# Kernel optimization log

Hardware: AMD Instinct MI355X
Metric: run time of the kernel (lower is better)

The kernel has to match this reference:

```python
import jax, jax.numpy as jnp
import numpy as np

H = 2048        # hidden_size
NH = 16         # num heads
QLR = 1536      # q_lora_rank
KVLR = 512      # kv_lora_rank
NOPE = 128      # qk_nope_head_dim
ROPE = 64       # qk_rope_head_dim
VH = 128        # v_head_dim
QHD = NOPE + ROPE
EPS = 1e-6
THETA = 10000.0


def rms_norm(x, w):
    x32 = x.astype(jnp.float32)
    inv = jax.lax.rsqrt(jnp.mean(x32 * x32, axis=-1, keepdims=True) + EPS)
    return (x32 * inv * w.astype(jnp.float32)).astype(x.dtype)


def rotate_half(x):
    h = x.shape[-1] // 2
    return jnp.concatenate([-x[..., h:], x[..., :h]], axis=-1)


def setup_inputs() -> dict:
    key = jax.random.key(0)
    ks = jax.random.split(key, 8)
    s = 0.02
    return {
        "hidden_states": jax.random.normal(ks[0], (1, 2048, H), dtype=jnp.float32),
        "q_a_w": jax.random.normal(ks[1], (QLR, H), dtype=jnp.float32) * s,
        "q_a_ln_w": jnp.ones((QLR,), dtype=jnp.float32),
        "q_b_w": jax.random.normal(ks[2], (NH * QHD, QLR), dtype=jnp.float32) * s,
        "kv_a_w": jax.random.normal(ks[3], (KVLR + ROPE, H), dtype=jnp.float32) * s,
        "kv_a_ln_w": jnp.ones((KVLR,), dtype=jnp.float32),
        "kv_b_w": jax.random.normal(ks[4], (NH * (NOPE + VH), KVLR), dtype=jnp.float32) * s,
        "o_w": jax.random.normal(ks[5], (H, NH * VH), dtype=jnp.float32) * s,
    }


def reference(hidden_states, q_a_w, q_a_ln_w, q_b_w, kv_a_w, kv_a_ln_w, kv_b_w, o_w):
    bsz, q_len, _ = hidden_states.shape
    scale = QHD ** -0.5

    # Q path: low-rank down-proj -> RMSNorm -> up-proj
    q_lat = rms_norm(hidden_states @ q_a_w.T, q_a_ln_w)
    q = (q_lat @ q_b_w.T).reshape(bsz, q_len, NH, QHD).transpose(0, 2, 1, 3)  # [B,H,S,QHD]
    q_nope, q_pe = q[..., :NOPE], q[..., NOPE:]

    # KV path: shared latent + decoupled rope key
    kv_lat_pe = hidden_states @ kv_a_w.T
    kv_lat, k_pe = kv_lat_pe[..., :KVLR], kv_lat_pe[..., KVLR:]
    k_pe = k_pe.reshape(bsz, q_len, 1, ROPE).transpose(0, 2, 1, 3)  # [B,1,S,R]
    kv = (rms_norm(kv_lat, kv_a_ln_w) @ kv_b_w.T).reshape(bsz, q_len, NH, NOPE + VH).transpose(0, 2, 1, 3)
    k_nope, v = kv[..., :NOPE], kv[..., NOPE:]

    # RoPE on decoupled sub-dim
    inv_freq = 1.0 / THETA ** (jnp.arange(0, ROPE, 2, dtype=jnp.float32) / ROPE)
    t = jnp.arange(q_len, dtype=jnp.float32)
    freqs = jnp.outer(t, inv_freq)
    emb = jnp.concatenate([freqs, freqs], axis=-1)
    cos = jnp.cos(emb)[None, None]  # [1,1,S,R]
    sin = jnp.sin(emb)[None, None]
    q_pe = q_pe * cos + rotate_half(q_pe) * sin
    k_pe = k_pe * cos + rotate_half(k_pe) * sin

    qs = jnp.concatenate([q_nope, q_pe], axis=-1)                                   # [B,H,S,QHD]
    ks = jnp.concatenate([k_nope, jnp.broadcast_to(k_pe, (bsz, NH, q_len, ROPE))], axis=-1)

    # causal SDPA
    scores = jnp.einsum('bhqd,bhkd->bhqk', qs, ks) * scale
    mask = jnp.tril(jnp.ones((q_len, q_len), dtype=bool))
    scores = jnp.where(mask[None, None], scores, jnp.finfo(scores.dtype).min)
    p = jax.nn.softmax(scores, axis=-1)
    attn = jnp.einsum('bhqk,bhkd->bhqd', p, v)

    attn = attn.transpose(0, 2, 1, 3).reshape(bsz, q_len, NH * VH)
    return attn @ o_w.T
```

## Files before the change

### kernel.cpp

```cpp
#include <hip/hip_runtime.h>
#include <cstdint>

#define H 2048
#define NH 16
#define QLR 1536
#define KVLR 512
#define NOPE 128
#define ROPED 64
#define VH 128
#define QHD 192
#define SEQ 2048
#define NQH (NH*QHD)
#define NKVC (NH*(NOPE+VH))
#define NOV (NH*VH)
#define KVAW_N (KVLR+ROPED)
#define SCALE_L2E 0.10411755f
#define NSEG 4

typedef __attribute__((ext_vector_type(8))) short short8;
typedef __attribute__((ext_vector_type(4))) short short4v;
typedef __attribute__((ext_vector_type(4))) float floatx4;

__device__ __forceinline__ short f2bf(float x) {
  unsigned u = __builtin_bit_cast(unsigned, x);
  unsigned r = (u + 0x7FFFu + ((u >> 16) & 1u)) >> 16;
  return (short)(unsigned short)r;
}
__device__ __forceinline__ float bf2f(short s) {
  unsigned u = ((unsigned)(unsigned short)s) << 16;
  return __builtin_bit_cast(float, u);
}
__device__ __forceinline__ void g2l16(const void* g, void* l) {
  __builtin_amdgcn_global_load_lds(
      (const __attribute__((address_space(1))) void*)(uintptr_t)(g),
      (__attribute__((address_space(3))) void*)(uintptr_t)(l),
      16, 0, 0);
}


struct CvtArgs {
  const float* src[6];
  short* dst[6];
  int cum[7];
};
__global__ __launch_bounds__(256) void k_cvt_all(CvtArgs a, int total4) {
  int stride = gridDim.x * 256;
  for (int i = blockIdx.x * 256 + threadIdx.x; i < total4; i += stride) {
    int j = 0;
#pragma unroll
    for (int t = 1; t < 6; ++t) j += (i >= a.cum[t]);
    int loc = i - a.cum[j];
    float4 v = ((const float4*)a.src[j])[loc];
    short4v o;
    o.x = f2bf(v.x); o.y = f2bf(v.y); o.z = f2bf(v.z); o.w = f2bf(v.w);
    ((short4v*)a.dst[j])[loc] = o;
  }
}

template<int EPI>
__global__ __launch_bounds__(256) void k_gemm128(
    const short* __restrict__ A, const short* __restrict__ B,
    float* __restrict__ C, float* __restrict__ C2, int N, int K)
{
  __shared__ short As[3][4096];
  __shared__ short Bs[3][4096];
  const int tid = threadIdx.x;
  const int lane = tid & 63;
  const int w = tid >> 6;
  const int wm = w & 1, wn = w >> 1;
  const int quad = lane >> 4, l16 = lane & 15;

  const int bid = blockIdx.x;
  const int xcd = bid & 7, j = bid >> 3;
  int mi_, ni_;
  if (EPI == 0) {
    mi_ = (xcd & 3) * 4 + (j & 3);
    ni_ = (xcd >> 2) * 8 + (j >> 2);
  } else {
    mi_ = (xcd & 3) * 4 + (j & 3);
    ni_ = (xcd >> 2) * 9 + (j >> 2);
    if (ni_ >= 17) return;
  }
  const int m0 = mi_ * 128, n0 = ni_ * 128;
  const int T = K >> 5;

  floatx4 acc[4][4] = {};

  auto issue = [&](int t, int buf) {
#pragma unroll
    for (int i = 0; i < 2; ++i) {
      int c = i*256 + tid;
      int row = c & 127, koct = c >> 7;
      g2l16(A + (size_t)(m0 + row)*K + t*32 + koct*8, As[buf] + (koct*128 + row)*8);
      g2l16(B + (size_t)(n0 + row)*K + t*32 + koct*8, Bs[buf] + (koct*128 + row)*8);
    }
  };

  issue(0, 0);
  issue(1, 1);
  int buf = 0;
  for (int t = 0; t < T; ++t) {
    if (t + 2 < T) {
      int nb = buf - 1; if (nb < 0) nb = 2;
      issue(t + 2, nb);
      asm volatile("s_waitcnt vmcnt(8)" ::: "memory");
    } else if (t + 1 < T) {
      asm volatile("s_waitcnt vmcnt(4)" ::: "memory");
    } else {
      asm volatile("s_waitcnt vmcnt(0)" ::: "memory");
    }
    asm volatile("s_barrier" ::: "memory");
    short8 af[4], bfr[4];
#pragma unroll
    for (int mi = 0; mi < 4; ++mi)
      af[mi] = *(const short8*)(As[buf] + (quad*128 + wm*64 + mi*16 + l16)*8);
#pragma unroll
    for (int ni = 0; ni < 4; ++ni)
      bfr[ni] = *(const short8*)(Bs[buf] + (quad*128 + wn*64 + ni*16 + l16)*8);
#pragma unroll
    for (int mi = 0; mi < 4; ++mi)
#pragma unroll
      for (int ni = 0; ni < 4; ++ni)
        acc[mi][ni] = __builtin_amdgcn_mfma_f32_16x16x32_bf16(af[mi], bfr[ni], acc[mi][ni], 0, 0, 0);
    asm volatile("s_barrier" ::: "memory");
    buf = buf + 1; if (buf > 2) buf = 0;
  }

#pragma unroll
  for (int mi = 0; mi < 4; ++mi) {
#pragma unroll
    for (int ni = 0; ni < 4; ++ni) {
      int col = n0 + wn*64 + ni*16 + l16;
#pragma unroll
      for (int r = 0; r < 4; ++r) {
        int row = m0 + wm*64 + mi*16 + quad*4 + r;
        if (EPI == 0) {
          C[(size_t)row*N + col] = acc[mi][ni][r];
        } else {
          if (col < QLR)                C[(size_t)row*QLR + col] = acc[mi][ni][r];
          else if (col < QLR + KVAW_N)  C2[(size_t)row*KVAW_N + (col - QLR)] = acc[mi][ni][r];
        }
      }
    }
  }
}

__global__ __launch_bounds__(256) void k_gemm2(
    const short* __restrict__ qlatn, const short* __restrict__ qbw,
    const short* __restrict__ kvln,  const short* __restrict__ kvbw,
    short* __restrict__ qhm, short* __restrict__ knope, short* __restrict__ vTd)
{
  __shared__ short As[3][4096];
  __shared__ short Bs[3][4096];
  const int tid = threadIdx.x;
  const int lane = tid & 63;
  const int w = tid >> 6;
  const int wm = w & 1, wn = w >> 1;
  const int quad = lane >> 4, l16 = lane & 15;
  int bid = blockIdx.x;
  const short *A, *B; int K, m0, n0; bool isq;
  if (bid < 384) {
    isq = true;  A = qlatn; B = qbw;  K = QLR;
    const int xcd = bid & 7, j = bid >> 3;
    m0 = ((xcd & 3) * 4 + (j & 3)) * 128;
    n0 = ((xcd >> 2) * 12 + (j >> 2)) * 128;
  } else {
    int b2 = bid - 384; isq = false; A = kvln; B = kvbw; K = KVLR;
    const int xcd = b2 & 7, j = b2 >> 3;
    m0 = ((xcd & 3) * 4 + (j & 3)) * 128;
    n0 = ((xcd >> 2) * 16 + (j >> 2)) * 128;
  }
  const int T = K >> 5;

  floatx4 acc[4][4] = {};

  auto issue = [&](int t, int buf) {
#pragma unroll
    for (int i = 0; i < 2; ++i) {
      int c = i*256 + tid;
      int row = c & 127, koct = c >> 7;
      g2l16(A + (size_t)(m0 + row)*K + t*32 + koct*8, As[buf] + (koct*128 + row)*8);
      g2l16(B + (size_t)(n0 + row)*K + t*32 + koct*8, Bs[buf] + (koct*128 + row)*8);
    }
  };

  issue(0, 0);
  issue(1, 1);
  int buf = 0;
  for (int t = 0; t < T; ++t) {
    if (t + 2 < T) {
      int nb = buf - 1; if (nb < 0) nb = 2;
      issue(t + 2, nb);
      asm volatile("s_waitcnt vmcnt(8)" ::: "memory");
    } else if (t + 1 < T) {
      asm volatile("s_waitcnt vmcnt(4)" ::: "memory");
    } else {
      asm volatile("s_waitcnt vmcnt(0)" ::: "memory");
    }
    asm volatile("s_barrier" ::: "memory");
    short8 af[4], bfr[4];
#pragma unroll
    for (int mi = 0; mi < 4; ++mi)
      af[mi] = *(const short8*)(As[buf] + (quad*128 + wm*64 + mi*16 + l16)*8);
#pragma unroll
    for (int ni = 0; ni < 4; ++ni)
      bfr[ni] = *(const short8*)(Bs[buf] + (quad*128 + wn*64 + ni*16 + l16)*8);
#pragma unroll
    for (int mi = 0; mi < 4; ++mi)
#pragma unroll
      for (int ni = 0; ni < 4; ++ni)
        acc[mi][ni] = __builtin_amdgcn_mfma_f32_16x16x32_bf16(af[mi], bfr[ni], acc[mi][ni], 0, 0, 0);
    asm volatile("s_barrier" ::: "memory");
    buf = buf + 1; if (buf > 2) buf = 0;
  }

  const int n064 = n0 + wn * 64;
  if (isq) {
    const int h = n064 / QHD;
    const bool ropew = (n064 % QHD) == 128;
    if (!ropew) {
      const int dbase = n064 - h * QHD;
#pragma unroll
      for (int mi = 0; mi < 4; ++mi) {
        const int qt = (m0 + wm*64 + mi*16) >> 4;
#pragma unroll
        for (int ni = 0; ni < 4; ++ni) {
          int d = dbase + ni*16 + l16;
          size_t tb = ((size_t)(h*128 + qt)*6 + (d>>5))*512
                    + (size_t)(((d>>3)&3)*16)*8 + (d&7);
#pragma unroll
          for (int r = 0; r < 4; ++r)
            qhm[tb + (quad*4 + r)*8] = f2bf(acc[mi][ni][r] * SCALE_L2E);
        }
      }
    } else {
#pragma unroll
      for (int ni = 0; ni < 2; ++ni) {
        int i = ni*16 + l16;
        float fr = powf(10000.0f, -(float)i / 32.0f);
        const int qoff = ((i>>3)*16)*8 + (i&7);
#pragma unroll
        for (int mi = 0; mi < 4; ++mi) {
          const int qt = (m0 + wm*64 + mi*16) >> 4;
          size_t t4 = ((size_t)(h*128 + qt)*6 + 4)*512 + qoff;
#pragma unroll
          for (int r = 0; r < 4; ++r) {
            int row = m0 + wm*64 + mi*16 + quad*4 + r;
            float ang = (float)row * fr;
            float cv, sv; __sincosf(ang, &sv, &cv);
            float x1 = acc[mi][ni][r], x2 = acc[mi][ni+2][r];
            qhm[t4 + (quad*4 + r)*8]       = f2bf((x1*cv - x2*sv) * SCALE_L2E);
            qhm[t4 + 512 + (quad*4 + r)*8] = f2bf((x2*cv + x1*sv) * SCALE_L2E);
          }
        }
      }
    }
  } else {
    const bool isv = (n064 & 128) != 0;
    if (!isv) {
#pragma unroll
      for (int mi = 0; mi < 4; ++mi) {
        const int kt = (m0 + wm*64 + mi*16) >> 4;
#pragma unroll
        for (int ni = 0; ni < 4; ++ni) {
          int col = n064 + ni*16 + l16;
          int hh = col >> 8, d = col & 127;
          size_t tb = ((size_t)(hh*128 + kt)*4 + (d>>5))*512
                    + (size_t)(((d>>3)&3)*16)*8 + (d&7);
#pragma unroll
          for (int r = 0; r < 4; ++r)
            knope[tb + (quad*4 + r)*8] = f2bf(acc[mi][ni][r]);
        }
      }
    } else {
#pragma unroll
      for (int mi = 0; mi < 4; ++mi) {
        const int row0 = m0 + wm*64 + mi*16 + quad*4;
        const int kb = row0 >> 5;
        const int voff = (((row0>>3)&3)*16)*8 + (row0 & 7);
#pragma unroll
        for (int ni = 0; ni < 4; ++ni) {
          int col = n064 + ni*16 + l16;
          int hh = col >> 8, dv = (col & 255) - 128;
          short4v pk;
          pk.x = f2bf(acc[mi][ni][0]); pk.y = f2bf(acc[mi][ni][1]);
          pk.z = f2bf(acc[mi][ni][2]); pk.w = f2bf(acc[mi][ni][3]);
          *(short4v*)(vTd + ((size_t)(hh*8 + (dv>>4))*64 + kb)*512
                          + voff + (dv & 15)*8) = pk;
        }
      }
    }
  }
}

__global__ __launch_bounds__(256) void k_rms2(
    const float* __restrict__ qlat, const float* __restrict__ q_a_ln,
    short* __restrict__ qlatn,
    const float* __restrict__ kvlp, const float* __restrict__ kv_a_ln,
    short* __restrict__ kvln, short* __restrict__ kpe)
{
  int b = blockIdx.x;
  __shared__ float red[4];
  if (b < SEQ) {
    int row = b;
    const float* xr = qlat + (size_t)row * QLR;
    float s = 0.f;
    for (int i = threadIdx.x; i < QLR; i += 256) { float v = xr[i]; s += v*v; }
#pragma unroll
    for (int off = 1; off < 64; off <<= 1) s += __shfl_xor(s, off);
    if ((threadIdx.x & 63) == 0) red[threadIdx.x >> 6] = s;
    __syncthreads();
    float inv = rsqrtf((red[0]+red[1]+red[2]+red[3]) / (float)QLR + 1e-6f);
    for (int i = threadIdx.x; i < QLR; i += 256)
      qlatn[(size_t)row * QLR + i] = f2bf(xr[i] * inv * q_a_ln[i]);
  } else {
    int row = b - SEQ;
    const float* xr = kvlp + (size_t)row * KVAW_N;
    float s = 0.f;
    for (int i = threadIdx.x; i < KVLR; i += 256) { float v = xr[i]; s += v*v; }
#pragma unroll
    for (int off = 1; off < 64; off <<= 1) s += __shfl_xor(s, off);
    if ((threadIdx.x & 63) == 0) red[threadIdx.x >> 6] = s;
    __syncthreads();
    float inv = rsqrtf((red[0]+red[1]+red[2]+red[3]) / (float)KVLR + 1e-6f);
    for (int i = threadIdx.x; i < KVLR; i += 256)
      kvln[(size_t)row * KVLR + i] = f2bf(xr[i] * inv * kv_a_ln[i]);
    if (threadIdx.x < 32) {
      int i = threadIdx.x;
      float ang = (float)row * powf(10000.0f, -(float)i / 32.0f);
      float cv, sv; __sincosf(ang, &sv, &cv);
      float x1 = xr[KVLR + i], x2 = xr[KVLR + 32 + i];
      size_t t0 = (size_t)((row >> 4) * 2) * 512
                + (size_t)(((i >> 3) * 16) + (row & 15)) * 8 + (i & 7);
      kpe[t0]       = f2bf(x1*cv - x2*sv);
      kpe[t0 + 512] = f2bf(x2*cv + x1*sv);
    }
  }
}

__device__ __constant__ unsigned char g_task[40] = {
  60,61,62,63, 56,57,58, 52,53,54, 48,49,50, 44,45,46,
  40,41, 36,37, 32,33, 28,29, 24, 20, 16, 12,
  59,42,25,8, 55,38,21,4, 51,34,17,0 };

__global__ __launch_bounds__(256) void k_attn8(
    const short* __restrict__ qhm,
    const short* __restrict__ knope,
    const short* __restrict__ kpe,
    const short* __restrict__ vT,
    short* __restrict__ Opart,
    float2* __restrict__ mlb)
{
  __shared__ short Ls[2][20480];
  __shared__ short Pl[4][32 * 72];
  const int tid = threadIdx.x;
  const int lane = tid & 63, w = tid >> 6;
  const int quad = lane >> 4, l16 = lane & 15;
  const int b = blockIdx.x;
  const int h = b & 15;
  const int qs2 = g_task[b >> 4];
  const int qb = qs2 >> 2, seg = qs2 & 3;
  const int cs = seg * 8;
  const int cend0 = 2 * qb + 2;
  const int cend = (cend0 < cs + 8) ? cend0 : (cs + 8);
  const int qws = qb * 128 + w * 32;
  short* Plw = Pl[w];

  const short* qbase = qhm   + (size_t)h * (128*6*512);
  const short* kbase = knope + (size_t)h * (128*4*512);
  const short* vbase = vT    + (size_t)h * (8*64*512);

  const int qt0 = qws >> 4;
  short8 qf[2][6];
#pragma unroll
  for (int nt = 0; nt < 2; ++nt)
#pragma unroll
    for (int ks = 0; ks < 6; ++ks)
      qf[nt][ks] = *(const short8*)(qbase + ((size_t)(qt0 + nt)*6 + ks)*512 + lane*8);

  auto issue = [&](int kc, int buf) {
    short* L = &Ls[buf][0];
    const short* ksrc = kbase + (size_t)kc * 8192;
    const short* psrc = kpe   + (size_t)kc * 4096;
#pragma unroll
    for (int i = 0; i < 4; ++i)
      g2l16(ksrc + (i*256 + tid)*8, L + (i*256 + tid)*8);
#pragma unroll
    for (int i = 0; i < 2; ++i)
      g2l16(psrc + (i*256 + tid)*8, L + 8192 + (i*256 + tid)*8);
#pragma unroll
    for (int i = 0; i < 4; ++i) {
      int uv = i*256 + tid;
      int dt = uv >> 7, wi = uv & 127;
      g2l16(vbase + ((size_t)(dt*64 + kc*2))*512 + wi*8, L + 12288 + uv*8);
    }
  };

  issue(cs, 0);
  if (cs + 1 < cend) issue(cs + 1, 1);

  floatx4 oacc[8][2] = {};
  float m_i[2] = {-1e30f, -1e30f}, l_i[2] = {0.f, 0.f};

  for (int kc = cs; kc < cend; ++kc) {
    if (kc + 1 < cend) asm volatile("s_waitcnt vmcnt(10)" ::: "memory");
    else               asm volatile("s_waitcnt vmcnt(0)" ::: "memory");
    asm volatile("s_barrier" ::: "memory");
    const short* Lb = &Ls[kc & 1][0];
    const int kv0 = kc * 64;

    floatx4 s[4][2] = {};
#pragma unroll
    for (int mt = 0; mt < 4; ++mt) {
      const short* kr = Lb + mt*2048 + lane*8;
      const short* pr = Lb + 8192 + mt*1024 + lane*8;
      short8 kf0 = *(const short8*)(kr);
      short8 kf1 = *(const short8*)(kr + 512);
      short8 kf2 = *(const short8*)(kr + 1024);
      short8 kf3 = *(const short8*)(kr + 1536);
      short8 kf4 = *(const short8*)(pr);
      short8 kf5 = *(const short8*)(pr + 512);
      s[mt][0] = __builtin_amdgcn_mfma_f32_16x16x32_bf16(kf0, qf[0][0], s[mt][0], 0, 0, 0);
      s[mt][1] = __builtin_amdgcn_mfma_f32_16x16x32_bf16(kf0, qf[1][0], s[mt][1], 0, 0, 0);
      s[mt][0] = __builtin_amdgcn_mfma_f32_16x16x32_bf16(kf1, qf[0][1], s[mt][0], 0, 0, 0);
      s[mt][1] = __builtin_amdgcn_mfma_f32_16x16x32_bf16(kf1, qf[1][1], s[mt][1], 0, 0, 0);
      s[mt][0] = __builtin_amdgcn_mfma_f32_16x16x32_bf16(kf2, qf[0][2], s[mt][0], 0, 0, 0);
      s[mt][1] = __builtin_amdgcn_mfma_f32_16x16x32_bf16(kf2, qf[1][2], s[mt][1], 0, 0, 0);
      s[mt][0] = __builtin_amdgcn_mfma_f32_16x16x32_bf16(kf3, qf[0][3], s[mt][0], 0, 0, 0);
      s[mt][1] = __builtin_amdgcn_mfma_f32_16x16x32_bf16(kf3, qf[1][3], s[mt][1], 0, 0, 0);
      s[mt][0] = __builtin_amdgcn_mfma_f32_16x16x32_bf16(kf4, qf[0][4], s[mt][0], 0, 0, 0);
      s[mt][1] = __builtin_amdgcn_mfma_f32_16x16x32_bf16(kf4, qf[1][4], s[mt][1], 0, 0, 0);
      s[mt][0] = __builtin_amdgcn_mfma_f32_16x16x32_bf16(kf5, qf[0][5], s[mt][0], 0, 0, 0);
      s[mt][1] = __builtin_amdgcn_mfma_f32_16x16x32_bf16(kf5, qf[1][5], s[mt][1], 0, 0, 0);
    }

    const bool diag = (kv0 + 64 > qws);
#pragma unroll
    for (int nt = 0; nt < 2; ++nt) {
      const int qg = qws + nt*16 + l16;
      float mx = -1e30f;
#pragma unroll
      for (int mt = 0; mt < 4; ++mt)
#pragma unroll
        for (int rr = 0; rr < 4; ++rr) {
          float v = s[mt][nt][rr];
          if (diag) {
            int kvg = kv0 + mt*16 + quad*4 + rr;
            v = (kvg <= qg) ? v : -1e30f;
            s[mt][nt][rr] = v;
          }
          mx = fmaxf(mx, v);
        }
      mx = fmaxf(mx, __shfl_xor(mx, 16));
      mx = fmaxf(mx, __shfl_xor(mx, 32));
      float mnew = fmaxf(m_i[nt], mx);
      float alpha = exp2f(m_i[nt] - mnew);
      m_i[nt] = mnew;
      float ssum = 0.f;
#pragma unroll
      for (int mt = 0; mt < 4; ++mt) {
        float p0 = exp2f(s[mt][nt][0] - mnew);
        float p1 = exp2f(s[mt][nt][1] - mnew);
        float p2 = exp2f(s[mt][nt][2] - mnew);
        float p3 = exp2f(s[mt][nt][3] - mnew);
        ssum += (p0 + p1) + (p2 + p3);
        short4v pk; pk.x = f2bf(p0); pk.y = f2bf(p1); pk.z = f2bf(p2); pk.w = f2bf(p3);
        *(short4v*)(Plw + (nt*16 + l16)*72 + mt*16 + quad*4) = pk;
      }
      ssum += __shfl_xor(ssum, 16);
      ssum += __shfl_xor(ssum, 32);
      l_i[nt] = l_i[nt] * alpha + ssum;
#pragma unroll
      for (int dt = 0; dt < 8; ++dt)
#pragma unroll
        for (int rr = 0; rr < 4; ++rr) oacc[dt][nt][rr] *= alpha;
    }

#pragma unroll
    for (int sl = 0; sl < 2; ++sl) {
      short8 pf0 = *(const short8*)(Plw + l16*72 + sl*32 + quad*8);
      short8 pf1 = *(const short8*)(Plw + (16 + l16)*72 + sl*32 + quad*8);
#pragma unroll
      for (int dt = 0; dt < 8; ++dt) {
        short8 vf = *(const short8*)(Lb + 12288 + (dt*2 + sl)*512 + lane*8);
        oacc[dt][0] = __builtin_amdgcn_mfma_f32_16x16x32_bf16(vf, pf0, oacc[dt][0], 0, 0, 0);
        oacc[dt][1] = __builtin_amdgcn_mfma_f32_16x16x32_bf16(vf, pf1, oacc[dt][1], 0, 0, 0);
      }
    }

    asm volatile("s_barrier" ::: "memory");
    if (kc + 2 < cend) issue(kc + 2, kc & 1);
  }

#pragma unroll
  for (int nt = 0; nt < 2; ++nt) {
    float inv = (l_i[nt] > 0.f) ? 1.f / l_i[nt] : 0.f;
    int q = qws + nt*16 + l16;
    if (quad == 0)
      mlb[((size_t)seg * SEQ + q) * NH + h] = make_float2(m_i[nt], l_i[nt]);
#pragma unroll
    for (int dt = 0; dt < 8; ++dt) {
      short4v pk;
      pk.x = f2bf(oacc[dt][nt][0] * inv);
      pk.y = f2bf(oacc[dt][nt][1] * inv);
      pk.z = f2bf(oacc[dt][nt][2] * inv);
      pk.w = f2bf(oacc[dt][nt][3] * inv);
      *(short4v*)(Opart + ((size_t)seg * SEQ + q) * NOV + h * VH + dt*16 + quad*4) = pk;
    }
  }
}

__global__ __launch_bounds__(256) void k_comb(
    const short* __restrict__ Opart, const float2* __restrict__ mlb,
    short* __restrict__ ob)
{
  int q = blockIdx.x;
  int hd0 = threadIdx.x * 8;
  int h = hd0 >> 7;
  int nact = (q >> 9) + 1;
  float2 mlv[NSEG];
  float M = -1e30f;
  for (int s = 0; s < nact; ++s) {
    mlv[s] = mlb[((size_t)s * SEQ + q) * NH + h];
    M = fmaxf(M, mlv[s].x);
  }
  float wgt[NSEG]; float L = 0.f;
  for (int s = 0; s < nact; ++s) {
    wgt[s] = mlv[s].y * exp2f(mlv[s].x - M);
    L += wgt[s];
  }
  float invL = 1.0f / L;
  float acc[8] = {};
  for (int s = 0; s < nact; ++s) {
    short8 o = *(const short8*)(Opart + ((size_t)s * SEQ + q) * NOV + hd0);
    float ws = wgt[s] * invL;
#pragma unroll
    for (int j = 0; j < 8; ++j) acc[j] += ws * bf2f(o[j]);
  }
  short8 rr;
#pragma unroll
  for (int j = 0; j < 8; ++j) rr[j] = f2bf(acc[j]);
  *(short8*)(ob + (size_t)q * NOV + hd0) = rr;
}

extern "C" void kernel_launch(void* const* d_in, const int* in_sizes, int n_in,
                              void* d_out, int out_size, void* d_ws, size_t ws_size,
                              hipStream_t stream) {
  const float* hs      = (const float*)d_in[0];
  const float* q_a_w   = (const float*)d_in[1];
  const float* q_a_ln  = (const float*)d_in[2];
  const float* q_b_w   = (const float*)d_in[3];
  const float* kv_a_w  = (const float*)d_in[4];
  const float* kv_a_ln = (const float*)d_in[5];
  const float* kv_b_w  = (const float*)d_in[6];
  const float* o_w     = (const float*)d_in[7];
  float* out = (float*)d_out;

  char* ws = (char*)d_ws;
  size_t off = 0;
  auto alloc = [&](size_t bytes) {
    void* p = ws + off;
    off += (bytes + 255) & ~(size_t)255;
    return p;
  };
  const size_t MB = 1u << 20;
  short* hs_b   = (short*)alloc((size_t)SEQ * H * 2);
  short* wab    = (short*)alloc((size_t)(QLR + KVAW_N + 64) * H * 2);
  short* qbw_b  = (short*)alloc((size_t)NQH * QLR * 2);
  short* kvbw_b = (short*)alloc((size_t)NKVC * KVLR * 2);
  short* ow_b   = (short*)alloc((size_t)H * NOV * 2);
  short* qhm    = (short*)alloc((size_t)NH * SEQ * QHD * 2);
  short* kpeb   = (short*)alloc((size_t)SEQ * ROPED * 2);
  short* knope  = (short*)alloc((size_t)NH * SEQ * NOPE * 2);
  short* vT     = (short*)alloc((size_t)NH * VH * SEQ * 2);
  short* attnb  = (short*)alloc((size_t)SEQ * NOV * 2);
  char* R = (char*)alloc(36 * MB);
  float* qlat  = (float*)R;
  short* qlatn = (short*)(R + 13 * MB);
  short* kvln  = (short*)(R + 20 * MB);
  float* kvlp  = (float*)(R + 24 * MB);
  short* Opart = (short*)R;
  float2* mlb  = (float2*)(R + 34 * MB);

  CvtArgs ca;
  ca.src[0] = hs;     ca.dst[0] = hs_b;
  ca.src[1] = q_a_w;  ca.dst[1] = wab;
  ca.src[2] = kv_a_w; ca.dst[2] = wab + (size_t)QLR * H;
  ca.src[3] = q_b_w;  ca.dst[3] = qbw_b;
  ca.src[4] = kv_b_w; ca.dst[4] = kvbw_b;
  ca.src[5] = o_w;    ca.dst[5] = ow_b;
  int sizes4[6] = { SEQ*H/4, QLR*H/4, KVAW_N*H/4, NQH*QLR/4, NKVC*KVLR/4, H*NOV/4 };
  ca.cum[0] = 0;
  for (int i = 0; i < 6; ++i) ca.cum[i+1] = ca.cum[i] + sizes4[i];
  k_cvt_all<<<2048, 256, 0, stream>>>(ca, ca.cum[6]);

  k_gemm128<1><<<288, 256, 0, stream>>>(
      hs_b, wab, qlat, kvlp, QLR + KVAW_N, H);
  k_rms2<<<2*SEQ, 256, 0, stream>>>(qlat, q_a_ln, qlatn, kvlp, kv_a_ln, kvln, kpeb);
  k_gemm2<<<896, 256, 0, stream>>>(qlatn, qbw_b, kvln, kvbw_b, qhm, knope, vT);
  k_attn8<<<640, 256, 0, stream>>>(qhm, knope, kpeb, vT, Opart, mlb);
  k_comb<<<SEQ, 256, 0, stream>>>(Opart, mlb, attnb);
  k_gemm128<0><<<256, 256, 0, stream>>>(
      attnb, ow_b, out, nullptr, H, NOV);
}
```

Before: 389.6 us.

## Split-K by two in projection GEMMs with atomic-add accumulation

Both k_gemm128 launches now split the K dimension in half, which doubles the grid (288→576 and 256→512 blocks) to fill more of the MI355X's CUs. Partial sums are accumulated into fp32 outputs via unsafeAtomicAdd, and three memsets zero the outputs beforehand. The XCD-to-tile mapping is reworked so each K-half pair lands on adjacent XCDs. The cost is atomic traffic on every output element plus the extra memsets, and the summation order becomes nondeterministic.

```diff
diff --git a/kernel.cpp b/kernel.cpp
--- a/kernel.cpp
+++ b/kernel.cpp
@@ -71,18 +71,23 @@
   const int quad = lane >> 4, l16 = lane & 15;
 
   const int bid = blockIdx.x;
-  const int xcd = bid & 7, j = bid >> 3;
+  const int xcd = bid & 7;
+  const int ks = xcd & 1;
+  const int q2 = xcd >> 1;
+  const int j = bid >> 3;
   int mi_, ni_;
   if (EPI == 0) {
-    mi_ = (xcd & 3) * 4 + (j & 3);
-    ni_ = (xcd >> 2) * 8 + (j >> 2);
+    mi_ = (q2 & 1) * 8 + (j & 7);
+    ni_ = (q2 >> 1) * 8 + (j >> 3);
   } else {
-    mi_ = (xcd & 3) * 4 + (j & 3);
-    ni_ = (xcd >> 2) * 9 + (j >> 2);
+    mi_ = (q2 & 1) * 8 + (j & 7);
+    ni_ = (q2 >> 1) * 9 + (j >> 3);
     if (ni_ >= 17) return;
   }
   const int m0 = mi_ * 128, n0 = ni_ * 128;
-  const int T = K >> 5;
+  const int KH = K >> 1;
+  const int k0 = ks * KH;
+  const int T = KH >> 5;
 
   floatx4 acc[4][4] = {};
 
@@ -91,8 +96,8 @@
     for (int i = 0; i < 2; ++i) {
       int c = i*256 + tid;
       int row = c & 127, koct = c >> 7;
-      g2l16(A + (size_t)(m0 + row)*K + t*32 + koct*8, As[buf] + (koct*128 + row)*8);
-      g2l16(B + (size_t)(n0 + row)*K + t*32 + koct*8, Bs[buf] + (koct*128 + row)*8);
+      g2l16(A + (size_t)(m0 + row)*K + k0 + t*32 + koct*8, As[buf] + (koct*128 + row)*8);
+      g2l16(B + (size_t)(n0 + row)*K + k0 + t*32 + koct*8, Bs[buf] + (koct*128 + row)*8);
     }
   };
 
@@ -135,10 +140,12 @@
       for (int r = 0; r < 4; ++r) {
         int row = m0 + wm*64 + mi*16 + quad*4 + r;
         if (EPI == 0) {
-          C[(size_t)row*N + col] = acc[mi][ni][r];
+          unsafeAtomicAdd(&C[(size_t)row*N + col], acc[mi][ni][r]);
         } else {
-          if (col < QLR)                C[(size_t)row*QLR + col] = acc[mi][ni][r];
-          else if (col < QLR + KVAW_N)  C2[(size_t)row*KVAW_N + (col - QLR)] = acc[mi][ni][r];
+          if (col < QLR)
+            unsafeAtomicAdd(&C[(size_t)row*QLR + col], acc[mi][ni][r]);
+          else if (col < QLR + KVAW_N)
+            unsafeAtomicAdd(&C2[(size_t)row*KVAW_N + (col - QLR)], acc[mi][ni][r]);
         }
       }
     }
@@ -582,6 +589,10 @@
   short* Opart = (short*)R;
   float2* mlb  = (float2*)(R + 34 * MB);
 
+  hipMemsetAsync(qlat, 0, (size_t)SEQ * QLR * 4, stream);
+  hipMemsetAsync(kvlp, 0, (size_t)SEQ * KVAW_N * 4, stream);
+  hipMemsetAsync(out,  0, (size_t)SEQ * H * 4, stream);
+
   CvtArgs ca;
   ca.src[0] = hs;     ca.dst[0] = hs_b;
   ca.src[1] = q_a_w;  ca.dst[1] = wab;
@@ -594,12 +605,12 @@
   for (int i = 0; i < 6; ++i) ca.cum[i+1] = ca.cum[i] + sizes4[i];
   k_cvt_all<<<2048, 256, 0, stream>>>(ca, ca.cum[6]);
 
-  k_gemm128<1><<<288, 256, 0, stream>>>(
+  k_gemm128<1><<<576, 256, 0, stream>>>(
       hs_b, wab, qlat, kvlp, QLR + KVAW_N, H);
   k_rms2<<<2*SEQ, 256, 0, stream>>>(qlat, q_a_ln, qlatn, kvlp, kv_a_ln, kvln, kpeb);
   k_gemm2<<<896, 256, 0, stream>>>(qlatn, qbw_b, kvln, kvbw_b, qhm, knope, vT);
   k_attn8<<<640, 256, 0, stream>>>(qhm, knope, kpeb, vT, Opart, mlb);
   k_comb<<<SEQ, 256, 0, stream>>>(Opart, mlb, attnb);
-  k_gemm128<0><<<256, 256, 0, stream>>>(
+  k_gemm128<0><<<512, 256, 0, stream>>>(
       attnb, ow_b, out, nullptr, H, NOV);
 }
```

After: 425.8 us. 9.3% more time.

## Split attention block into 8 waves of 16 query rows and add lazy rescaling

Applied to the files above, without the earlier changes.

The attention kernel now launches 512 threads per block, with each wave owning 16 query rows instead of 32. This halves per-wave accumulator registers and spreads the shared K/V tile loads across twice as many threads. It also adds a conditional online-softmax rescale: when the running max rises by no more than 8 in log2 space across the whole wave, the max and accumulator rescale are skipped. The trade-off is that the K/V LDS tiles are reused by fewer MFMA N-tiles per wave, and the skipped rescale lets exp2 values grow up to 2^8, which could affect bf16 precision of P.

```diff
diff --git a/kernel.cpp b/kernel.cpp
--- a/kernel.cpp
+++ b/kernel.cpp
@@ -343,7 +343,7 @@
   40,41, 36,37, 32,33, 28,29, 24, 20, 16, 12,
   59,42,25,8, 55,38,21,4, 51,34,17,0 };
 
-__global__ __launch_bounds__(256) void k_attn8(
+__global__ __launch_bounds__(512) void k_attn8(
     const short* __restrict__ qhm,
     const short* __restrict__ knope,
     const short* __restrict__ kpe,
@@ -352,7 +352,7 @@
     float2* __restrict__ mlb)
 {
   __shared__ short Ls[2][20480];
-  __shared__ short Pl[4][32 * 72];
+  __shared__ short Pl[8][16 * 72];
   const int tid = threadIdx.x;
   const int lane = tid & 63, w = tid >> 6;
   const int quad = lane >> 4, l16 = lane & 15;
@@ -363,7 +363,7 @@
   const int cs = seg * 8;
   const int cend0 = 2 * qb + 2;
   const int cend = (cend0 < cs + 8) ? cend0 : (cs + 8);
-  const int qws = qb * 128 + w * 32;
+  const int qws = qb * 128 + w * 16;
   short* Plw = Pl[w];
 
   const short* qbase = qhm   + (size_t)h * (128*6*512);
@@ -371,26 +371,22 @@
   const short* vbase = vT    + (size_t)h * (8*64*512);
 
   const int qt0 = qws >> 4;
-  short8 qf[2][6];
-#pragma unroll
-  for (int nt = 0; nt < 2; ++nt)
-#pragma unroll
-    for (int ks = 0; ks < 6; ++ks)
-      qf[nt][ks] = *(const short8*)(qbase + ((size_t)(qt0 + nt)*6 + ks)*512 + lane*8);
+  short8 qf[6];
+#pragma unroll
+  for (int ks = 0; ks < 6; ++ks)
+    qf[ks] = *(const short8*)(qbase + ((size_t)qt0*6 + ks)*512 + lane*8);
 
   auto issue = [&](int kc, int buf) {
     short* L = &Ls[buf][0];
     const short* ksrc = kbase + (size_t)kc * 8192;
     const short* psrc = kpe   + (size_t)kc * 4096;
 #pragma unroll
-    for (int i = 0; i < 4; ++i)
-      g2l16(ksrc + (i*256 + tid)*8, L + (i*256 + tid)*8);
-#pragma unroll
     for (int i = 0; i < 2; ++i)
-      g2l16(psrc + (i*256 + tid)*8, L + 8192 + (i*256 + tid)*8);
-#pragma unroll
-    for (int i = 0; i < 4; ++i) {
-      int uv = i*256 + tid;
+      g2l16(ksrc + (i*512 + tid)*8, L + (i*512 + tid)*8);
+    g2l16(psrc + tid*8, L + 8192 + tid*8);
+#pragma unroll
+    for (int i = 0; i < 2; ++i) {
+      int uv = i*512 + tid;
       int dt = uv >> 7, wi = uv & 127;
       g2l16(vbase + ((size_t)(dt*64 + kc*2))*512 + wi*8, L + 12288 + uv*8);
     }
@@ -399,17 +395,17 @@
   issue(cs, 0);
   if (cs + 1 < cend) issue(cs + 1, 1);
 
-  floatx4 oacc[8][2] = {};
-  float m_i[2] = {-1e30f, -1e30f}, l_i[2] = {0.f, 0.f};
+  floatx4 oacc[8] = {};
+  float m_i = -1e30f, l_i = 0.f;
 
   for (int kc = cs; kc < cend; ++kc) {
-    if (kc + 1 < cend) asm volatile("s_waitcnt vmcnt(10)" ::: "memory");
+    if (kc + 1 < cend) asm volatile("s_waitcnt vmcnt(5)" ::: "memory");
     else               asm volatile("s_waitcnt vmcnt(0)" ::: "memory");
     asm volatile("s_barrier" ::: "memory");
     const short* Lb = &Ls[kc & 1][0];
     const int kv0 = kc * 64;
 
-    floatx4 s[4][2] = {};
+    floatx4 s[4] = {};
 #pragma unroll
     for (int mt = 0; mt < 4; ++mt) {
       const short* kr = Lb + mt*2048 + lane*8;
@@ -420,71 +416,66 @@
       short8 kf3 = *(const short8*)(kr + 1536);
       short8 kf4 = *(const short8*)(pr);
       short8 kf5 = *(const short8*)(pr + 512);
-      s[mt][0] = __builtin_amdgcn_mfma_f32_16x16x32_bf16(kf0, qf[0][0], s[mt][0], 0, 0, 0);
-      s[mt][1] = __builtin_amdgcn_mfma_f32_16x16x32_bf16(kf0, qf[1][0], s[mt][1], 0, 0, 0);
-      s[mt][0] = __builtin_amdgcn_mfma_f32_16x16x32_bf16(kf1, qf[0][1], s[mt][0], 0, 0, 0);
-      s[mt][1] = __builtin_amdgcn_mfma_f32_16x16x32_bf16(kf1, qf[1][1], s[mt][1], 0, 0, 0);
-      s[mt][0] = __builtin_amdgcn_mfma_f32_16x16x32_bf16(kf2, qf[0][2], s[mt][0], 0, 0, 0);
-      s[mt][1] = __builtin_amdgcn_mfma_f32_16x16x32_bf16(kf2, qf[1][2], s[mt][1], 0, 0, 0);
-      s[mt][0] = __builtin_amdgcn_mfma_f32_16x16x32_bf16(kf3, qf[0][3], s[mt][0], 0, 0, 0);
-      s[mt][1] = __builtin_amdgcn_mfma_f32_16x16x32_bf16(kf3, qf[1][3], s[mt][1], 0, 0, 0);
-      s[mt][0] = __builtin_amdgcn_mfma_f32_16x16x32_bf16(kf4, qf[0][4], s[mt][0], 0, 0, 0);
-      s[mt][1] = __builtin_amdgcn_mfma_f32_16x16x32_bf16(kf4, qf[1][4], s[mt][1], 0, 0, 0);
-      s[mt][0] = __builtin_amdgcn_mfma_f32_16x16x32_bf16(kf5, qf[0][5], s[mt][0], 0, 0, 0);
-      s[mt][1] = __builtin_amdgcn_mfma_f32_16x16x32_bf16(kf5, qf[1][5], s[mt][1], 0, 0, 0);
+      s[mt] = __builtin_amdgcn_mfma_f32_16x16x32_bf16(kf0, qf[0], s[mt], 0, 0, 0);
+      s[mt] = __builtin_amdgcn_mfma_f32_16x16x32_bf16(kf1, qf[1], s[mt], 0, 0, 0);
+      s[mt] = __builtin_amdgcn_mfma_f32_16x16x32_bf16(kf2, qf[2], s[mt], 0, 0, 0);
+      s[mt] = __builtin_amdgcn_mfma_f32_16x16x32_bf16(kf3, qf[3], s[mt], 0, 0, 0);
+      s[mt] = __builtin_amdgcn_mfma_f32_16x16x32_bf16(kf4, qf[4], s[mt], 0, 0, 0);
+      s[mt] = __builtin_amdgcn_mfma_f32_16x16x32_bf16(kf5, qf[5], s[mt], 0, 0, 0);
     }
 
     const bool diag = (kv0 + 64 > qws);
-#pragma unroll
-    for (int nt = 0; nt < 2; ++nt) {
-      const int qg = qws + nt*16 + l16;
-      float mx = -1e30f;
-#pragma unroll
-      for (int mt = 0; mt < 4; ++mt)
-#pragma unroll
-        for (int rr = 0; rr < 4; ++rr) {
-          float v = s[mt][nt][rr];
-          if (diag) {
-            int kvg = kv0 + mt*16 + quad*4 + rr;
-            v = (kvg <= qg) ? v : -1e30f;
-            s[mt][nt][rr] = v;
-          }
-          mx = fmaxf(mx, v);
+    const int qg = qws + l16;
+    float mx = -1e30f;
+#pragma unroll
+    for (int mt = 0; mt < 4; ++mt)
+#pragma unroll
+      for (int rr = 0; rr < 4; ++rr) {
+        float v = s[mt][rr];
+        if (diag) {
+          int kvg = kv0 + mt*16 + quad*4 + rr;
+          v = (kvg <= qg) ? v : -1e30f;
+          s[mt][rr] = v;
         }
-      mx = fmaxf(mx, __shfl_xor(mx, 16));
-      mx = fmaxf(mx, __shfl_xor(mx, 32));
-      float mnew = fmaxf(m_i[nt], mx);
-      float alpha = exp2f(m_i[nt] - mnew);
-      m_i[nt] = mnew;
-      float ssum = 0.f;
-#pragma unroll
-      for (int mt = 0; mt < 4; ++mt) {
-        float p0 = exp2f(s[mt][nt][0] - mnew);
-        float p1 = exp2f(s[mt][nt][1] - mnew);
-        float p2 = exp2f(s[mt][nt][2] - mnew);
-        float p3 = exp2f(s[mt][nt][3] - mnew);
-        ssum += (p0 + p1) + (p2 + p3);
-        short4v pk; pk.x = f2bf(p0); pk.y = f2bf(p1); pk.z = f2bf(p2); pk.w = f2bf(p3);
-        *(short4v*)(Plw + (nt*16 + l16)*72 + mt*16 + quad*4) = pk;
-      }
-      ssum += __shfl_xor(ssum, 16);
-      ssum += __shfl_xor(ssum, 32);
-      l_i[nt] = l_i[nt] * alpha + ssum;
+        mx = fmaxf(mx, v);
+      }
+    mx = fmaxf(mx, __shfl_xor(mx, 16));
+    mx = fmaxf(mx, __shfl_xor(mx, 32));
+    const bool skip = __all(mx - m_i <= 8.0f);
+    float alpha = 1.0f;
+    if (!skip) {
+      float mnew = fmaxf(m_i, mx);
+      alpha = exp2f(m_i - mnew);
+      m_i = mnew;
+    }
+    float ssum = 0.f;
+#pragma unroll
+    for (int mt = 0; mt < 4; ++mt) {
+      float p0 = exp2f(s[mt][0] - m_i);
+      float p1 = exp2f(s[mt][1] - m_i);
+      float p2 = exp2f(s[mt][2] - m_i);
+      float p3 = exp2f(s[mt][3] - m_i);
+      ssum += (p0 + p1) + (p2 + p3);
+      short4v pk; pk.x = f2bf(p0); pk.y = f2bf(p1); pk.z = f2bf(p2); pk.w = f2bf(p3);
+      *(short4v*)(Plw + l16*72 + mt*16 + quad*4) = pk;
+    }
+    ssum += __shfl_xor(ssum, 16);
+    ssum += __shfl_xor(ssum, 32);
+    l_i = l_i * alpha + ssum;
+    if (!skip) {
 #pragma unroll
       for (int dt = 0; dt < 8; ++dt)
 #pragma unroll
-        for (int rr = 0; rr < 4; ++rr) oacc[dt][nt][rr] *= alpha;
+        for (int rr = 0; rr < 4; ++rr) oacc[dt][rr] *= alpha;
     }
 
 #pragma unroll
     for (int sl = 0; sl < 2; ++sl) {
-      short8 pf0 = *(const short8*)(Plw + l16*72 + sl*32 + quad*8);
-      short8 pf1 = *(const short8*)(Plw + (16 + l16)*72 + sl*32 + quad*8);
+      short8 pf = *(const short8*)(Plw + l16*72 + sl*32 + quad*8);
 #pragma unroll
       for (int dt = 0; dt < 8; ++dt) {
         short8 vf = *(const short8*)(Lb + 12288 + (dt*2 + sl)*512 + lane*8);
-        oacc[dt][0] = __builtin_amdgcn_mfma_f32_16x16x32_bf16(vf, pf0, oacc[dt][0], 0, 0, 0);
-        oacc[dt][1] = __builtin_amdgcn_mfma_f32_16x16x32_bf16(vf, pf1, oacc[dt][1], 0, 0, 0);
+        oacc[dt] = __builtin_amdgcn_mfma_f32_16x16x32_bf16(vf, pf, oacc[dt], 0, 0, 0);
       }
     }
 
@@ -492,19 +483,18 @@
     if (kc + 2 < cend) issue(kc + 2, kc & 1);
   }
 
-#pragma unroll
-  for (int nt = 0; nt < 2; ++nt) {
-    float inv = (l_i[nt] > 0.f) ? 1.f / l_i[nt] : 0.f;
-    int q = qws + nt*16 + l16;
+  {
+    float inv = (l_i > 0.f) ? 1.f / l_i : 0.f;
+    int q = qws + l16;
     if (quad == 0)
-      mlb[((size_t)seg * SEQ + q) * NH + h] = make_float2(m_i[nt], l_i[nt]);
+      mlb[((size_t)seg * SEQ + q) * NH + h] = make_float2(m_i, l_i);
 #pragma unroll
     for (int dt = 0; dt < 8; ++dt) {
       short4v pk;
-      pk.x = f2bf(oacc[dt][nt][0] * inv);
-      pk.y = f2bf(oacc[dt][nt][1] * inv);
-      pk.z = f2bf(oacc[dt][nt][2] * inv);
-      pk.w = f2bf(oacc[dt][nt][3] * inv);
+      pk.x = f2bf(oacc[dt][0] * inv);
+      pk.y = f2bf(oacc[dt][1] * inv);
+      pk.z = f2bf(oacc[dt][2] * inv);
+      pk.w = f2bf(oacc[dt][3] * inv);
       *(short4v*)(Opart + ((size_t)seg * SEQ + q) * NOV + h * VH + dt*16 + quad*4) = pk;
     }
   }
@@ -598,7 +588,7 @@
       hs_b, wab, qlat, kvlp, QLR + KVAW_N, H);
   k_rms2<<<2*SEQ, 256, 0, stream>>>(qlat, q_a_ln, qlatn, kvlp, kv_a_ln, kvln, kpeb);
   k_gemm2<<<896, 256, 0, stream>>>(qlatn, qbw_b, kvln, kvbw_b, qhm, knope, vT);
-  k_attn8<<<640, 256, 0, stream>>>(qhm, knope, kpeb, vT, Opart, mlb);
+  k_attn8<<<640, 512, 0, stream>>>(qhm, knope, kpeb, vT, Opart, mlb);
   k_comb<<<SEQ, 256, 0, stream>>>(Opart, mlb, attnb);
   k_gemm128<0><<<256, 256, 0, stream>>>(
       attnb, ow_b, out, nullptr, H, NOV);
```

New measurement: 386.3 us, median of 2. No clear change (-0.8%).
